# Kernel tuning notes

Measured on AMD Instinct MI355X. Metric: run time of the kernel, lower is better.

The kernel has to match this reference:

```python
import jax, jax.numpy as jnp
import numpy as np

N_NODES = 100000
N_EDGES = 1600000
N_GRAPHS = 200
NODES_PER_GRAPH = N_NODES // N_GRAPHS
IN_DIM, HID, LAT = 24, 64, 32


def setup_inputs() -> dict:
    key = jax.random.key(0)
    ks = jax.random.split(key, 12)
    x = jax.random.normal(ks[0], (N_NODES, IN_DIM), jnp.float32)
    edge_index = jax.random.randint(ks[1], (2, N_EDGES), 0, N_NODES, jnp.int32)
    batch = (jnp.arange(N_NODES, dtype=jnp.int32) // NODES_PER_GRAPH)
    eps = jax.random.normal(ks[2], (N_GRAPHS, LAT), jnp.float32)

    def lin(k, i, o):
        s = 1.0 / np.sqrt(i)
        return jax.random.uniform(k, (i, o), jnp.float32, -s, s)

    return {
        "x": x, "edge_index": edge_index, "batch": batch, "eps": eps,
        "W1": lin(ks[3], IN_DIM, HID), "b1": jnp.zeros((HID,), jnp.float32),
        "W2": lin(ks[4], HID, HID), "b2": jnp.zeros((HID,), jnp.float32),
        "Wmu": lin(ks[5], HID, LAT), "bmu": jnp.zeros((LAT,), jnp.float32),
        "Wlv": lin(ks[6], HID, LAT), "blv": jnp.zeros((LAT,), jnp.float32),
        "Wd1": lin(ks[7], LAT, 128), "bd1": jnp.zeros((128,), jnp.float32),
        "Wd2": lin(ks[8], 128, IN_DIM), "bd2": jnp.zeros((IN_DIM,), jnp.float32),
        "num_nodes_per_graph": NODES_PER_GRAPH,
        "num_graphs": N_GRAPHS,
    }


def gcn_conv(x, edge_index, W, b, n_nodes):
    # PyG GCNConv: linear transform, add self-loops, symmetric normalization,
    # scatter-add aggregation at target (col) nodes, then bias.
    h = x @ W  # [N, out]
    loops = jnp.arange(n_nodes, dtype=edge_index.dtype)
    row = jnp.concatenate([edge_index[0], loops])  # source nodes
    col = jnp.concatenate([edge_index[1], loops])  # target nodes
    deg = jax.ops.segment_sum(jnp.ones_like(col, h.dtype), col, n_nodes)
    dinv = jnp.where(deg > 0, jax.lax.rsqrt(deg), 0.0)
    norm = dinv[row] * dinv[col]  # [E+N]
    msg = h[row] * norm[:, None]  # gather + scale (memory-bound)
    out = jax.ops.segment_sum(msg, col, n_nodes)  # scatter-add
    return out + b


def reference(x, edge_index, batch, eps, W1, b1, W2, b2, Wmu, bmu, Wlv, blv,
              Wd1, bd1, Wd2, bd2, num_nodes_per_graph, num_graphs):
    n_nodes = x.shape[0]
    h = jax.nn.relu(gcn_conv(x, edge_index, W1, b1, n_nodes))
    h = jax.nn.relu(gcn_conv(h, edge_index, W2, b2, n_nodes))
    # global mean pool over graphs
    sums = jax.ops.segment_sum(h, batch, num_graphs)
    cnt = jax.ops.segment_sum(jnp.ones((n_nodes,), h.dtype), batch, num_graphs)
    pooled = sums / jnp.maximum(cnt, 1.0)[:, None]
    mu = pooled @ Wmu + bmu
    logvar = pooled @ Wlv + blv
    # reparameterize with provided eps (torch.randn_like surrogate)
    z = mu + eps * jnp.exp(0.5 * logvar)
    # decoder: repeat each z num_nodes_per_graph times
    z_exp = jnp.repeat(z, num_nodes_per_graph, axis=0)  # [G*nn, LAT]
    hd = jax.nn.relu(z_exp @ Wd1 + bd1)
    recon_x = jax.nn.sigmoid(hd @ Wd2 + bd2)
    return recon_x, mu, logvar
```

## Files before the change

### kernel.cpp

```cpp
#include <hip/hip_runtime.h>
#include <hip/hip_bf16.h>
#include <hip/hip_fp8.h>

constexpr int N_NODES = 100000;
constexpr int N_EDGES = 1600000;
constexpr int N_GRAPHS = 200;
constexpr int NPG = 500;
constexpr int IN_DIM = 24;
constexpr int HID = 64;
constexpr int LAT = 32;
constexpr int DEC = 128;
constexpr int CAP = 48;
constexpr int P2 = 512;
constexpr int NPP = 196;
constexpr int PART_CAP = 3840;
constexpr int KP_BLOCKS = 200;
constexpr int KP_CHUNK = N_EDGES / KP_BLOCKS;

typedef __attribute__((ext_vector_type(8))) short short8;
typedef __attribute__((ext_vector_type(4))) float f32x4;
typedef __attribute__((ext_vector_type(2))) float f32x2;

constexpr int OFF_CNT = 0;
constexpr int OFF_GCOUNT = 100000;
constexpr int OFF_ROWS = 102400;
constexpr int OFF_A = OFF_ROWS + N_NODES * CAP;
constexpr int OFF_B = OFF_A + N_NODES * HID / 2;
constexpr int OFF_HS1 = OFF_B + N_NODES * HID / 2;
constexpr int OFF_PARTIAL = OFF_HS1 + (N_NODES + 1) * 16;

__global__ __launch_bounds__(1024) void k_part(const int* __restrict__ ei,
                                               int* __restrict__ gcount,
                                               unsigned int* __restrict__ epart) {
    __shared__ int hist[P2];
    __shared__ int ptrs[P2];
    int t = threadIdx.x;
    for (int i = t; i < P2; i += 1024) hist[i] = 0;
    __syncthreads();
    int e0 = blockIdx.x * KP_CHUNK;
    const int4* cols4 = reinterpret_cast<const int4*>(ei + N_EDGES + e0);
    const int4* rows4 = reinterpret_cast<const int4*>(ei + e0);
    for (int i = t; i < KP_CHUNK / 4; i += 1024) {
        int4 c = cols4[i];
        atomicAdd(&hist[c.x / NPP], 1);
        atomicAdd(&hist[c.y / NPP], 1);
        atomicAdd(&hist[c.z / NPP], 1);
        atomicAdd(&hist[c.w / NPP], 1);
    }
    __syncthreads();
    for (int i = t; i < P2; i += 1024) ptrs[i] = atomicAdd(gcount + i, hist[i]);
    __syncthreads();
    for (int i = t; i < KP_CHUNK / 4; i += 1024) {
        int4 c = cols4[i];
        int4 r = rows4[i];
#pragma unroll
        for (int k = 0; k < 4; ++k) {
            int cc = (k == 0) ? c.x : (k == 1) ? c.y : (k == 2) ? c.z : c.w;
            int rr = (k == 0) ? r.x : (k == 1) ? r.y : (k == 2) ? r.z : r.w;
            int p = cc / NPP;
            int cl = cc - p * NPP;
            int pos = atomicAdd(&ptrs[p], 1);
            if (pos < PART_CAP)
                epart[p * PART_CAP + pos] = ((unsigned)cl << 17) | (unsigned)rr;
        }
    }
}

__device__ inline unsigned char f2fp8(float f) {
    __hip_fp8_e4m3 v(f);
    return (unsigned char)v.__x;
}

__device__ inline unsigned short f2bf(float f) {
    __hip_bfloat16 h = __float2bfloat16(f);
    return *reinterpret_cast<unsigned short*>(&h);
}

__global__ __launch_bounds__(256) void k_fill3_lin1(
    const unsigned int* __restrict__ epart, const int* __restrict__ gcount,
    const float* __restrict__ x, const float* __restrict__ W1,
    int* __restrict__ cnt, int* __restrict__ rows,
    unsigned char* __restrict__ HS1) {
    __shared__ int lcnt[NPP];
    __shared__ int lrows[NPP * CAP];
    __shared__ float Ws[IN_DIM * HID];
    int p = blockIdx.x, t = threadIdx.x;
    if (p == 0 && t < 16)
        reinterpret_cast<unsigned int*>(HS1)[N_NODES * 16 + t] = 0;
    for (int i = t; i < NPP; i += 256) lcnt[i] = 0;
    for (int i = t; i < IN_DIM * HID; i += 256) Ws[i] = W1[i];
    __syncthreads();
    int m = min(gcount[p], PART_CAP);
    for (int i = t; i < m; i += 256) {
        unsigned v = epart[p * PART_CAP + i];
        int cl = v >> 17;
        int r = (int)(v & 0x1FFFFu);
        int pos = atomicAdd(&lcnt[cl], 1);
        if (pos < CAP) lrows[cl * CAP + pos] = r;
    }
    __syncthreads();
    int node0 = p * NPP;
    int nn = min(NPP, N_NODES - node0);
    if (nn <= 0) return;
    for (int i = t; i < nn * CAP; i += 256) rows[node0 * CAP + i] = lrows[i];
    for (int i = t; i < nn; i += 256) cnt[node0 + i] = lcnt[i];
    __syncthreads();
    float* xs = reinterpret_cast<float*>(lrows);
    for (int i = t; i < nn * IN_DIM; i += 256) xs[i] = x[node0 * IN_DIM + i];
    __syncthreads();
    for (int o = t; o < nn * HID; o += 256) {
        int j = o >> 6, col = o & 63;
        float acc = 0.f;
#pragma unroll
        for (int k = 0; k < IN_DIM; ++k) acc += xs[j * IN_DIM + k] * Ws[k * HID + col];
        float dinv = rsqrtf((float)(lcnt[j] + 1));
        HS1[(node0 + j) * HID + col] = f2fp8(acc * dinv);
    }
}

__device__ inline void acc_fp8x4p(unsigned int u, f32x2& lo, f32x2& hi) {
    lo += __builtin_amdgcn_cvt_pk_f32_fp8(u, false);
    hi += __builtin_amdgcn_cvt_pk_f32_fp8(u, true);
}

__device__ inline void gatherT(int base, int lane,
                               const int* __restrict__ cnt,
                               const int* __restrict__ rows,
                               const unsigned char* __restrict__ HS,
                               f32x2& lo, f32x2& hi, int& cn_out) {
    int fq = lane & 15, rs = lane >> 4;
    const unsigned int* HSq = reinterpret_cast<const unsigned int*>(HS);
    int node = base + rs;
    int cn = __builtin_nontemporal_load(cnt + node);
    int np = min(cn, CAP);
    int mx = np;
    mx = max(mx, __shfl_xor(mx, 16, 64));
    mx = max(mx, __shfl_xor(mx, 32, 64));
    const int* rb = rows + node * CAP;
    int idx0 = (fq < np)      ? __builtin_nontemporal_load(rb + fq)      : N_NODES;
    int idx1 = (16 + fq < np) ? __builtin_nontemporal_load(rb + 16 + fq) : N_NODES;
    int idx2 = (32 + fq < np) ? __builtin_nontemporal_load(rb + 32 + fq) : N_NODES;
    f32x2 z = {0.f, 0.f};
    lo = z; hi = z;
    acc_fp8x4p(HSq[node * 16 + fq], lo, hi);
    int rbase = rs * 16;
    {
        unsigned int u[32];
#pragma unroll
        for (int c = 0; c < 16; ++c) {
            int r = __shfl(idx0, rbase + c, 64);
            u[c] = HSq[r * 16 + fq];
        }
#pragma unroll
        for (int c = 0; c < 16; ++c) {
            int r = __shfl(idx1, rbase + c, 64);
            u[16 + c] = HSq[r * 16 + fq];
        }
#pragma unroll
        for (int c = 0; c < 32; ++c) acc_fp8x4p(u[c], lo, hi);
    }
    if (mx > 32) {
        unsigned int u[16];
#pragma unroll
        for (int c = 0; c < 16; ++c) {
            int r = __shfl(idx2, rbase + c, 64);
            u[c] = HSq[r * 16 + fq];
        }
#pragma unroll
        for (int c = 0; c < 16; ++c) acc_fp8x4p(u[c], lo, hi);
    }
    cn_out = cn;
}

__global__ __launch_bounds__(256) void k_gather1mm(
    const int* __restrict__ cnt, const int* __restrict__ rows,
    const unsigned char* __restrict__ HS1, const float* __restrict__ b1,
    const float* __restrict__ W2, unsigned char* __restrict__ HS2) {
    __shared__ unsigned short W2T[HID * 72];
    __shared__ unsigned short H1s[16 * 72];
    __shared__ float dinvL[16];
    int tid = threadIdx.x;
    if (blockIdx.x == 0 && tid < 16)
        reinterpret_cast<unsigned int*>(HS2)[N_NODES * 16 + tid] = 0;
    for (int i = tid; i < HID * HID; i += 256) {
        int k = i >> 6, n = i & 63;
        W2T[n * 72 + k] = f2bf(W2[i]);
    }
    int wave = tid >> 6, lane = tid & 63;
    int fq = lane & 15, rs = lane >> 4;
    int base = blockIdx.x * 16 + wave * 4;
    f32x2 lo, hi;
    int cn;
    gatherT(base, lane, cnt, rows, HS1, lo, hi, cn);
    float dinv = rsqrtf((float)(cn + 1));
    float4 bv = reinterpret_cast<const float4*>(b1)[fq];
    int r = wave * 4 + rs;
    ushort4 o;
    o.x = f2bf(fmaxf(dinv * lo.x + bv.x, 0.f));
    o.y = f2bf(fmaxf(dinv * lo.y + bv.y, 0.f));
    o.z = f2bf(fmaxf(dinv * hi.x + bv.z, 0.f));
    o.w = f2bf(fmaxf(dinv * hi.y + bv.w, 0.f));
    *reinterpret_cast<ushort4*>(&H1s[r * 72 + fq * 4]) = o;
    if (fq == 0) dinvL[r] = dinv;
    __syncthreads();
    int m = lane & 15, quad = lane >> 4;
    short8 a0 = *reinterpret_cast<const short8*>(&H1s[m * 72 + quad * 8]);
    short8 a1 = *reinterpret_cast<const short8*>(&H1s[m * 72 + 32 + quad * 8]);
    short8 b0 = *reinterpret_cast<const short8*>(&W2T[(wave * 16 + m) * 72 + quad * 8]);
    short8 b1v = *reinterpret_cast<const short8*>(&W2T[(wave * 16 + m) * 72 + 32 + quad * 8]);
    f32x4 acc = {0.f, 0.f, 0.f, 0.f};
    acc = __builtin_amdgcn_mfma_f32_16x16x32_bf16(a0, b0, acc, 0, 0, 0);
    acc = __builtin_amdgcn_mfma_f32_16x16x32_bf16(a1, b1v, acc, 0, 0, 0);
    int row0 = blockIdx.x * 16;
#pragma unroll
    for (int reg = 0; reg < 4; ++reg) {
        int rr = quad * 4 + reg;
        HS2[(row0 + rr) * HID + wave * 16 + m] = f2fp8(acc[reg] * dinvL[rr]);
    }
}

__global__ __launch_bounds__(256) void k_gather2(const int* __restrict__ cnt,
                                                 const int* __restrict__ rows,
                                                 const unsigned char* __restrict__ HS2,
                                                 const float* __restrict__ b2,
                                                 float* __restrict__ partial) {
    int tid = threadIdx.x;
    int wave = tid >> 6, lane = tid & 63;
    int w = blockIdx.x * 4 + wave;
    int base = w * 4;
    f32x2 lo, hi;
    int cn;
    gatherT(base, lane, cnt, rows, HS2, lo, hi, cn);
    int fq = lane & 15, rs = lane >> 4;
    float dinv = rsqrtf((float)(cn + 1));
    float4 bv = reinterpret_cast<const float4*>(b2)[fq];
    f32x4 h;
    h.x = fmaxf(dinv * lo.x + bv.x, 0.f);
    h.y = fmaxf(dinv * lo.y + bv.y, 0.f);
    h.z = fmaxf(dinv * hi.x + bv.z, 0.f);
    h.w = fmaxf(dinv * hi.y + bv.w, 0.f);
    h.x += __shfl_xor(h.x, 16, 64); h.x += __shfl_xor(h.x, 32, 64);
    h.y += __shfl_xor(h.y, 16, 64); h.y += __shfl_xor(h.y, 32, 64);
    h.z += __shfl_xor(h.z, 16, 64); h.z += __shfl_xor(h.z, 32, 64);
    h.w += __shfl_xor(h.w, 16, 64); h.w += __shfl_xor(h.w, 32, 64);
    if (rs == 0)
        __builtin_nontemporal_store(h, reinterpret_cast<f32x4*>(partial + w * HID) + fq);
}

__global__ __launch_bounds__(128) void k_head_bcast(
    const float* __restrict__ partial, const float* __restrict__ eps,
    const float* __restrict__ Wmu, const float* __restrict__ bmu,
    const float* __restrict__ Wlv, const float* __restrict__ blv,
    const float* __restrict__ Wd1, const float* __restrict__ bd1,
    const float* __restrict__ Wd2, const float* __restrict__ bd2,
    float* __restrict__ out_mu, float* __restrict__ out_lv,
    float* __restrict__ out_recon) {
    int g = blockIdx.x, tid = threadIdx.x;
    __shared__ float p[HID];
    __shared__ float zs[LAT];
    __shared__ float hds[DEC];
    __shared__ __align__(16) float rg[IN_DIM];
    if (tid < HID) {
        float s = 0.f;
#pragma unroll 5
        for (int r = 0; r < NPG / 4; ++r)
            s += partial[(g * (NPG / 4) + r) * HID + tid];
        p[tid] = s * (1.0f / NPG);
    }
    __syncthreads();
    if (tid < LAT) {
        float m = bmu[tid], l = blv[tid];
#pragma unroll 8
        for (int k = 0; k < HID; ++k) {
            m += p[k] * Wmu[k * LAT + tid];
            l += p[k] * Wlv[k * LAT + tid];
        }
        out_mu[g * LAT + tid] = m;
        out_lv[g * LAT + tid] = l;
        zs[tid] = m + eps[g * LAT + tid] * expf(0.5f * l);
    }
    __syncthreads();
    {
        float a = bd1[tid];
#pragma unroll 8
        for (int k = 0; k < LAT; ++k) a += zs[k] * Wd1[k * DEC + tid];
        hds[tid] = fmaxf(a, 0.f);
    }
    __syncthreads();
    if (tid < IN_DIM) {
        float a = bd2[tid];
#pragma unroll 8
        for (int k = 0; k < DEC; ++k) a += hds[k] * Wd2[k * IN_DIM + tid];
        rg[tid] = 1.0f / (1.0f + expf(-a));
    }
    __syncthreads();
    const float4* rg4 = reinterpret_cast<const float4*>(rg);
    float4* dst = reinterpret_cast<float4*>(out_recon + g * NPG * IN_DIM);
    for (int j = tid; j < NPG * IN_DIM / 4; j += 128) dst[j] = rg4[j % (IN_DIM / 4)];
}

extern "C" void kernel_launch(void* const* d_in, const int* in_sizes, int n_in,
                              void* d_out, int out_size, void* d_ws, size_t ws_size,
                              hipStream_t stream) {
    const float* x = (const float*)d_in[0];
    const int* ei = (const int*)d_in[1];
    const float* eps = (const float*)d_in[3];
    const float* W1 = (const float*)d_in[4];
    const float* b1 = (const float*)d_in[5];
    const float* W2 = (const float*)d_in[6];
    const float* b2 = (const float*)d_in[7];
    const float* Wmu = (const float*)d_in[8];
    const float* bmu = (const float*)d_in[9];
    const float* Wlv = (const float*)d_in[10];
    const float* blv = (const float*)d_in[11];
    const float* Wd1 = (const float*)d_in[12];
    const float* bd1 = (const float*)d_in[13];
    const float* Wd2 = (const float*)d_in[14];
    const float* bd2 = (const float*)d_in[15];

    float* ws = (float*)d_ws;
    int* cnt = (int*)ws + OFF_CNT;
    int* gcount = (int*)ws + OFF_GCOUNT;
    int* rows = (int*)ws + OFF_ROWS;
    unsigned int* epart = (unsigned int*)((int*)ws + OFF_A);
    unsigned char* HS1 = (unsigned char*)((int*)ws + OFF_HS1);
    unsigned char* HS2 = (unsigned char*)((int*)ws + OFF_A);
    float* partial = ws + OFF_PARTIAL;

    float* out = (float*)d_out;
    float* out_recon = out;
    float* out_mu = out + N_NODES * IN_DIM;
    float* out_lv = out_mu + N_GRAPHS * LAT;

    hipMemsetAsync(gcount, 0, P2 * sizeof(int), stream);

    k_part<<<KP_BLOCKS, 1024, 0, stream>>>(ei, gcount, epart);
    k_fill3_lin1<<<P2, 256, 0, stream>>>(epart, gcount, x, W1, cnt, rows, HS1);

    k_gather1mm<<<N_NODES / 16, 256, 0, stream>>>(cnt, rows, HS1, b1, W2, HS2);

    k_gather2<<<N_NODES / 16, 256, 0, stream>>>(cnt, rows, HS2, b2, partial);

    k_head_bcast<<<N_GRAPHS, 128, 0, stream>>>(partial, eps, Wmu, bmu, Wlv, blv,
                                               Wd1, bd1, Wd2, bd2, out_mu,
                                               out_lv, out_recon);
}
```

Baseline: 205.4 us.

## Split fp8 feature tables into column halves and separate layer-2 GEMM

Stores the fp8 hidden feature tables as two 32-column halves so each gather pass touches a 32-byte row. Each half is gathered by its own block (interleaved by blockIdx), with 8 lanes per node and 8 nodes per wave. The first gather no longer does the W2 matmul; it writes a bf16 H1 buffer, and a new MFMA GEMM kernel produces the split layer-2 tables. The head kernel is widened to 256 threads so the partial reduction runs on four segments. This trades an extra launch and an H1 round trip for a smaller per-pass random-access footprint that is intended to stay resident in cache.

```diff
diff --git a/kernel.cpp b/kernel.cpp
--- a/kernel.cpp
+++ b/kernel.cpp
@@ -80,13 +80,15 @@
     const unsigned int* __restrict__ epart, const int* __restrict__ gcount,
     const float* __restrict__ x, const float* __restrict__ W1,
     int* __restrict__ cnt, int* __restrict__ rows,
-    unsigned char* __restrict__ HS1) {
+    unsigned char* __restrict__ HS1a, unsigned char* __restrict__ HS1b) {
     __shared__ int lcnt[NPP];
     __shared__ int lrows[NPP * CAP];
     __shared__ float Ws[IN_DIM * HID];
     int p = blockIdx.x, t = threadIdx.x;
-    if (p == 0 && t < 16)
-        reinterpret_cast<unsigned int*>(HS1)[N_NODES * 16 + t] = 0;
+    if (p == 0 && t < 8) {
+        reinterpret_cast<unsigned int*>(HS1a)[N_NODES * 8 + t] = 0;
+        reinterpret_cast<unsigned int*>(HS1b)[N_NODES * 8 + t] = 0;
+    }
     for (int i = t; i < NPP; i += 256) lcnt[i] = 0;
     for (int i = t; i < IN_DIM * HID; i += 256) Ws[i] = W1[i];
     __syncthreads();
@@ -114,7 +116,9 @@
 #pragma unroll
         for (int k = 0; k < IN_DIM; ++k) acc += xs[j * IN_DIM + k] * Ws[k * HID + col];
         float dinv = rsqrtf((float)(lcnt[j] + 1));
-        HS1[(node0 + j) * HID + col] = f2fp8(acc * dinv);
+        unsigned char v = f2fp8(acc * dinv);
+        if (col < 32) HS1a[(node0 + j) * 32 + col] = v;
+        else          HS1b[(node0 + j) * 32 + col - 32] = v;
     }
 }
 
@@ -123,131 +127,163 @@
     hi += __builtin_amdgcn_cvt_pk_f32_fp8(u, true);
 }
 
-__device__ inline void gatherT(int base, int lane,
-                               const int* __restrict__ cnt,
-                               const int* __restrict__ rows,
-                               const unsigned char* __restrict__ HS,
-                               f32x2& lo, f32x2& hi, int& cn_out) {
-    int fq = lane & 15, rs = lane >> 4;
+__device__ inline void gatherT8(int base, int lane,
+                                const int* __restrict__ cnt,
+                                const int* __restrict__ rows,
+                                const unsigned char* __restrict__ HS,
+                                f32x2& lo, f32x2& hi, int& cn_out) {
+    int fq = lane & 7, rs = lane >> 3;
     const unsigned int* HSq = reinterpret_cast<const unsigned int*>(HS);
     int node = base + rs;
     int cn = __builtin_nontemporal_load(cnt + node);
     int np = min(cn, CAP);
     int mx = np;
+    mx = max(mx, __shfl_xor(mx, 8, 64));
     mx = max(mx, __shfl_xor(mx, 16, 64));
     mx = max(mx, __shfl_xor(mx, 32, 64));
     const int* rb = rows + node * CAP;
     int idx0 = (fq < np)      ? __builtin_nontemporal_load(rb + fq)      : N_NODES;
-    int idx1 = (16 + fq < np) ? __builtin_nontemporal_load(rb + 16 + fq) : N_NODES;
-    int idx2 = (32 + fq < np) ? __builtin_nontemporal_load(rb + 32 + fq) : N_NODES;
+    int idx1 = (8 + fq < np)  ? __builtin_nontemporal_load(rb + 8 + fq)  : N_NODES;
+    int idx2 = (16 + fq < np) ? __builtin_nontemporal_load(rb + 16 + fq) : N_NODES;
+    int idx3 = (24 + fq < np) ? __builtin_nontemporal_load(rb + 24 + fq) : N_NODES;
     f32x2 z = {0.f, 0.f};
     lo = z; hi = z;
-    acc_fp8x4p(HSq[node * 16 + fq], lo, hi);
-    int rbase = rs * 16;
+    acc_fp8x4p(HSq[node * 8 + fq], lo, hi);
+    int rbase = rs * 8;
     {
         unsigned int u[32];
 #pragma unroll
-        for (int c = 0; c < 16; ++c) {
-            int r = __shfl(idx0, rbase + c, 64);
-            u[c] = HSq[r * 16 + fq];
-        }
-#pragma unroll
-        for (int c = 0; c < 16; ++c) {
-            int r = __shfl(idx1, rbase + c, 64);
-            u[16 + c] = HSq[r * 16 + fq];
-        }
+        for (int c = 0; c < 8; ++c) { int r = __shfl(idx0, rbase + c, 64); u[c] = HSq[r * 8 + fq]; }
+#pragma unroll
+        for (int c = 0; c < 8; ++c) { int r = __shfl(idx1, rbase + c, 64); u[8 + c] = HSq[r * 8 + fq]; }
+#pragma unroll
+        for (int c = 0; c < 8; ++c) { int r = __shfl(idx2, rbase + c, 64); u[16 + c] = HSq[r * 8 + fq]; }
+#pragma unroll
+        for (int c = 0; c < 8; ++c) { int r = __shfl(idx3, rbase + c, 64); u[24 + c] = HSq[r * 8 + fq]; }
 #pragma unroll
         for (int c = 0; c < 32; ++c) acc_fp8x4p(u[c], lo, hi);
     }
     if (mx > 32) {
+        int idx4 = (32 + fq < np) ? __builtin_nontemporal_load(rb + 32 + fq) : N_NODES;
+        int idx5 = (40 + fq < np) ? __builtin_nontemporal_load(rb + 40 + fq) : N_NODES;
         unsigned int u[16];
 #pragma unroll
-        for (int c = 0; c < 16; ++c) {
-            int r = __shfl(idx2, rbase + c, 64);
-            u[c] = HSq[r * 16 + fq];
-        }
+        for (int c = 0; c < 8; ++c) { int r = __shfl(idx4, rbase + c, 64); u[c] = HSq[r * 8 + fq]; }
+#pragma unroll
+        for (int c = 0; c < 8; ++c) { int r = __shfl(idx5, rbase + c, 64); u[8 + c] = HSq[r * 8 + fq]; }
 #pragma unroll
         for (int c = 0; c < 16; ++c) acc_fp8x4p(u[c], lo, hi);
     }
     cn_out = cn;
 }
 
-__global__ __launch_bounds__(256) void k_gather1mm(
-    const int* __restrict__ cnt, const int* __restrict__ rows,
-    const unsigned char* __restrict__ HS1, const float* __restrict__ b1,
-    const float* __restrict__ W2, unsigned char* __restrict__ HS2) {
-    __shared__ unsigned short W2T[HID * 72];
-    __shared__ unsigned short H1s[16 * 72];
-    __shared__ float dinvL[16];
+__global__ __launch_bounds__(256) void k_gather1s(const int* __restrict__ cnt,
+                                                  const int* __restrict__ rows,
+                                                  const unsigned char* __restrict__ HS1a,
+                                                  const unsigned char* __restrict__ HS1b,
+                                                  const float* __restrict__ b1,
+                                                  unsigned short* __restrict__ H1) {
     int tid = threadIdx.x;
-    if (blockIdx.x == 0 && tid < 16)
-        reinterpret_cast<unsigned int*>(HS2)[N_NODES * 16 + tid] = 0;
-    for (int i = tid; i < HID * HID; i += 256) {
-        int k = i >> 6, n = i & 63;
-        W2T[n * 72 + k] = f2bf(W2[i]);
-    }
+    int h = blockIdx.x & 1;
+    int nb = blockIdx.x >> 1;
     int wave = tid >> 6, lane = tid & 63;
-    int fq = lane & 15, rs = lane >> 4;
-    int base = blockIdx.x * 16 + wave * 4;
+    int base = nb * 32 + wave * 8;
+    const unsigned char* HS = h ? HS1b : HS1a;
     f32x2 lo, hi;
     int cn;
-    gatherT(base, lane, cnt, rows, HS1, lo, hi, cn);
+    gatherT8(base, lane, cnt, rows, HS, lo, hi, cn);
+    int fq = lane & 7, rs = lane >> 3;
     float dinv = rsqrtf((float)(cn + 1));
-    float4 bv = reinterpret_cast<const float4*>(b1)[fq];
-    int r = wave * 4 + rs;
+    float4 bv = reinterpret_cast<const float4*>(b1)[h * 8 + fq];
     ushort4 o;
     o.x = f2bf(fmaxf(dinv * lo.x + bv.x, 0.f));
     o.y = f2bf(fmaxf(dinv * lo.y + bv.y, 0.f));
     o.z = f2bf(fmaxf(dinv * hi.x + bv.z, 0.f));
     o.w = f2bf(fmaxf(dinv * hi.y + bv.w, 0.f));
-    *reinterpret_cast<ushort4*>(&H1s[r * 72 + fq * 4]) = o;
-    if (fq == 0) dinvL[r] = dinv;
-    __syncthreads();
+    *reinterpret_cast<ushort4*>(H1 + (base + rs) * HID + h * 32 + fq * 4) = o;
+}
+
+__global__ __launch_bounds__(256) void k_gemm2(const unsigned short* __restrict__ H1,
+                                               const float* __restrict__ W2,
+                                               const int* __restrict__ cnt,
+                                               unsigned char* __restrict__ HS2a,
+                                               unsigned char* __restrict__ HS2b) {
+    __shared__ unsigned short W2T[HID * 72];
+    int tid = threadIdx.x;
+    if (blockIdx.x == 0 && tid < 8) {
+        reinterpret_cast<unsigned int*>(HS2a)[N_NODES * 8 + tid] = 0;
+        reinterpret_cast<unsigned int*>(HS2b)[N_NODES * 8 + tid] = 0;
+    }
+    for (int i = tid; i < HID * HID; i += 256) {
+        int k = i >> 6, n = i & 63;
+        W2T[n * 72 + k] = f2bf(W2[i]);
+    }
+    __syncthreads();
+    int wave = tid >> 6, lane = tid & 63;
+    int wid = blockIdx.x * 4 + wave;
+    if (wid >= N_NODES / 16) return;
+    int row0 = wid * 16;
     int m = lane & 15, quad = lane >> 4;
-    short8 a0 = *reinterpret_cast<const short8*>(&H1s[m * 72 + quad * 8]);
-    short8 a1 = *reinterpret_cast<const short8*>(&H1s[m * 72 + 32 + quad * 8]);
-    short8 b0 = *reinterpret_cast<const short8*>(&W2T[(wave * 16 + m) * 72 + quad * 8]);
-    short8 b1v = *reinterpret_cast<const short8*>(&W2T[(wave * 16 + m) * 72 + 32 + quad * 8]);
-    f32x4 acc = {0.f, 0.f, 0.f, 0.f};
-    acc = __builtin_amdgcn_mfma_f32_16x16x32_bf16(a0, b0, acc, 0, 0, 0);
-    acc = __builtin_amdgcn_mfma_f32_16x16x32_bf16(a1, b1v, acc, 0, 0, 0);
-    int row0 = blockIdx.x * 16;
-#pragma unroll
-    for (int reg = 0; reg < 4; ++reg) {
-        int rr = quad * 4 + reg;
-        HS2[(row0 + rr) * HID + wave * 16 + m] = f2fp8(acc[reg] * dinvL[rr]);
-    }
-}
-
-__global__ __launch_bounds__(256) void k_gather2(const int* __restrict__ cnt,
-                                                 const int* __restrict__ rows,
-                                                 const unsigned char* __restrict__ HS2,
-                                                 const float* __restrict__ b2,
-                                                 float* __restrict__ partial) {
+    const short8* Av = reinterpret_cast<const short8*>(H1);
+    short8 a0 = Av[(row0 + m) * 8 + quad];
+    short8 a1 = Av[(row0 + m) * 8 + 4 + quad];
+    float dv[4];
+#pragma unroll
+    for (int reg = 0; reg < 4; ++reg)
+        dv[reg] = rsqrtf((float)(cnt[row0 + quad * 4 + reg] + 1));
+#pragma unroll
+    for (int nt = 0; nt < 4; ++nt) {
+        short8 b0 = *reinterpret_cast<const short8*>(&W2T[(nt * 16 + m) * 72 + quad * 8]);
+        short8 b1v = *reinterpret_cast<const short8*>(&W2T[(nt * 16 + m) * 72 + 32 + quad * 8]);
+        f32x4 acc = {0.f, 0.f, 0.f, 0.f};
+        acc = __builtin_amdgcn_mfma_f32_16x16x32_bf16(a0, b0, acc, 0, 0, 0);
+        acc = __builtin_amdgcn_mfma_f32_16x16x32_bf16(a1, b1v, acc, 0, 0, 0);
+        int col = nt * 16 + m;
+#pragma unroll
+        for (int reg = 0; reg < 4; ++reg) {
+            int r = row0 + quad * 4 + reg;
+            unsigned char v = f2fp8(acc[reg] * dv[reg]);
+            if (col < 32) HS2a[r * 32 + col] = v;
+            else          HS2b[r * 32 + col - 32] = v;
+        }
+    }
+}
+
+__global__ __launch_bounds__(256) void k_gather2s(const int* __restrict__ cnt,
+                                                  const int* __restrict__ rows,
+                                                  const unsigned char* __restrict__ HS2a,
+                                                  const unsigned char* __restrict__ HS2b,
+                                                  const float* __restrict__ b2,
+                                                  float* __restrict__ partial) {
     int tid = threadIdx.x;
+    int h = blockIdx.x & 1;
+    int nb = blockIdx.x >> 1;
     int wave = tid >> 6, lane = tid & 63;
-    int w = blockIdx.x * 4 + wave;
-    int base = w * 4;
+    int base = nb * 32 + wave * 8;
+    const unsigned char* HS = h ? HS2b : HS2a;
     f32x2 lo, hi;
     int cn;
-    gatherT(base, lane, cnt, rows, HS2, lo, hi, cn);
-    int fq = lane & 15, rs = lane >> 4;
+    gatherT8(base, lane, cnt, rows, HS, lo, hi, cn);
+    int fq = lane & 7, rs = lane >> 3;
     float dinv = rsqrtf((float)(cn + 1));
-    float4 bv = reinterpret_cast<const float4*>(b2)[fq];
-    f32x4 h;
-    h.x = fmaxf(dinv * lo.x + bv.x, 0.f);
-    h.y = fmaxf(dinv * lo.y + bv.y, 0.f);
-    h.z = fmaxf(dinv * hi.x + bv.z, 0.f);
-    h.w = fmaxf(dinv * hi.y + bv.w, 0.f);
-    h.x += __shfl_xor(h.x, 16, 64); h.x += __shfl_xor(h.x, 32, 64);
-    h.y += __shfl_xor(h.y, 16, 64); h.y += __shfl_xor(h.y, 32, 64);
-    h.z += __shfl_xor(h.z, 16, 64); h.z += __shfl_xor(h.z, 32, 64);
-    h.w += __shfl_xor(h.w, 16, 64); h.w += __shfl_xor(h.w, 32, 64);
-    if (rs == 0)
-        __builtin_nontemporal_store(h, reinterpret_cast<f32x4*>(partial + w * HID) + fq);
-}
-
-__global__ __launch_bounds__(128) void k_head_bcast(
+    float4 bv = reinterpret_cast<const float4*>(b2)[h * 8 + fq];
+    f32x4 hv;
+    hv.x = fmaxf(dinv * lo.x + bv.x, 0.f);
+    hv.y = fmaxf(dinv * lo.y + bv.y, 0.f);
+    hv.z = fmaxf(dinv * hi.x + bv.z, 0.f);
+    hv.w = fmaxf(dinv * hi.y + bv.w, 0.f);
+    hv.x += __shfl_xor(hv.x, 8, 64);  hv.x += __shfl_xor(hv.x, 16, 64);
+    hv.y += __shfl_xor(hv.y, 8, 64);  hv.y += __shfl_xor(hv.y, 16, 64);
+    hv.z += __shfl_xor(hv.z, 8, 64);  hv.z += __shfl_xor(hv.z, 16, 64);
+    hv.w += __shfl_xor(hv.w, 8, 64);  hv.w += __shfl_xor(hv.w, 16, 64);
+    if (rs == 0 || rs == 4) {
+        int w = (base >> 2) + (rs >> 2);
+        __builtin_nontemporal_store(
+            hv, reinterpret_cast<f32x4*>(partial + w * HID + h * 32) + fq);
+    }
+}
+
+__global__ __launch_bounds__(256) void k_head_bcast(
     const float* __restrict__ partial, const float* __restrict__ eps,
     const float* __restrict__ Wmu, const float* __restrict__ bmu,
     const float* __restrict__ Wlv, const float* __restrict__ blv,
@@ -256,17 +292,21 @@
     float* __restrict__ out_mu, float* __restrict__ out_lv,
     float* __restrict__ out_recon) {
     int g = blockIdx.x, tid = threadIdx.x;
+    __shared__ float ps[4][HID];
     __shared__ float p[HID];
     __shared__ float zs[LAT];
     __shared__ float hds[DEC];
     __shared__ __align__(16) float rg[IN_DIM];
-    if (tid < HID) {
+    {
+        int col = tid & 63, seg = tid >> 6;
         float s = 0.f;
-#pragma unroll 5
-        for (int r = 0; r < NPG / 4; ++r)
-            s += partial[(g * (NPG / 4) + r) * HID + tid];
-        p[tid] = s * (1.0f / NPG);
-    }
+        for (int r = seg; r < NPG / 4; r += 4)
+            s += partial[(g * (NPG / 4) + r) * HID + col];
+        ps[seg][col] = s;
+    }
+    __syncthreads();
+    if (tid < HID)
+        p[tid] = (ps[0][tid] + ps[1][tid] + ps[2][tid] + ps[3][tid]) * (1.0f / NPG);
     __syncthreads();
     if (tid < LAT) {
         float m = bmu[tid], l = blv[tid];
@@ -280,7 +320,7 @@
         zs[tid] = m + eps[g * LAT + tid] * expf(0.5f * l);
     }
     __syncthreads();
-    {
+    if (tid < DEC) {
         float a = bd1[tid];
 #pragma unroll 8
         for (int k = 0; k < LAT; ++k) a += zs[k] * Wd1[k * DEC + tid];
@@ -296,7 +336,7 @@
     __syncthreads();
     const float4* rg4 = reinterpret_cast<const float4*>(rg);
     float4* dst = reinterpret_cast<float4*>(out_recon + g * NPG * IN_DIM);
-    for (int j = tid; j < NPG * IN_DIM / 4; j += 128) dst[j] = rg4[j % (IN_DIM / 4)];
+    for (int j = tid; j < NPG * IN_DIM / 4; j += 256) dst[j] = rg4[j % (IN_DIM / 4)];
 }
 
 extern "C" void kernel_launch(void* const* d_in, const int* in_sizes, int n_in,
@@ -323,8 +363,11 @@
     int* gcount = (int*)ws + OFF_GCOUNT;
     int* rows = (int*)ws + OFF_ROWS;
     unsigned int* epart = (unsigned int*)((int*)ws + OFF_A);
-    unsigned char* HS1 = (unsigned char*)((int*)ws + OFF_HS1);
-    unsigned char* HS2 = (unsigned char*)((int*)ws + OFF_A);
+    unsigned short* H1 = (unsigned short*)((int*)ws + OFF_B);
+    unsigned char* HS1a = (unsigned char*)((int*)ws + OFF_HS1);
+    unsigned char* HS1b = HS1a + (N_NODES + 1) * 32;
+    unsigned char* HS2a = (unsigned char*)((int*)ws + OFF_A);
+    unsigned char* HS2b = HS2a + (N_NODES + 1) * 32;
     float* partial = ws + OFF_PARTIAL;
 
     float* out = (float*)d_out;
@@ -335,13 +378,14 @@
     hipMemsetAsync(gcount, 0, P2 * sizeof(int), stream);
 
     k_part<<<KP_BLOCKS, 1024, 0, stream>>>(ei, gcount, epart);
-    k_fill3_lin1<<<P2, 256, 0, stream>>>(epart, gcount, x, W1, cnt, rows, HS1);
-
-    k_gather1mm<<<N_NODES / 16, 256, 0, stream>>>(cnt, rows, HS1, b1, W2, HS2);
-
-    k_gather2<<<N_NODES / 16, 256, 0, stream>>>(cnt, rows, HS2, b2, partial);
-
-    k_head_bcast<<<N_GRAPHS, 128, 0, stream>>>(partial, eps, Wmu, bmu, Wlv, blv,
+    k_fill3_lin1<<<P2, 256, 0, stream>>>(epart, gcount, x, W1, cnt, rows, HS1a, HS1b);
+
+    k_gather1s<<<2 * (N_NODES / 32), 256, 0, stream>>>(cnt, rows, HS1a, HS1b, b1, H1);
+    k_gemm2<<<(N_NODES / 16 + 3) / 4, 256, 0, stream>>>(H1, W2, cnt, HS2a, HS2b);
+
+    k_gather2s<<<2 * (N_NODES / 32), 256, 0, stream>>>(cnt, rows, HS2a, HS2b, b2, partial);
+
+    k_head_bcast<<<N_GRAPHS, 256, 0, stream>>>(partial, eps, Wmu, bmu, Wlv, blv,
                                                Wd1, bd1, Wd2, bd2, out_mu,
                                                out_lv, out_recon);
 }
```

Result: slower. 228.6 us (+11.3%).
